# Kernel optimization log

Hardware: AMD Instinct MI355X
Metric: run time of the kernel (lower is better)

The kernel has to match this reference:

```python
import math
import jax, jax.numpy as jnp
import numpy as np

B, S, D, H = 4, 2048, 1024, 16

def setup_inputs() -> dict:
    key = jax.random.key(0)
    k1, k2, k3 = jax.random.split(key, 3)
    scale_in = 1.0 / math.sqrt(D)
    return {
        "x": jax.random.normal(k1, (B, S, D), dtype=jnp.float32),
        "w_in": jax.random.normal(k2, (D, 3 * D), dtype=jnp.float32) * scale_in,
        "b_in": jnp.zeros((3 * D,), dtype=jnp.float32),
        "w_out": jax.random.normal(k3, (D, D), dtype=jnp.float32) * scale_in,
        "b_out": jnp.zeros((D,), dtype=jnp.float32),
    }

def reference(x, w_in, b_in, w_out, b_out):
    b, s, d = x.shape
    hd = d // H  # head dim
    qkv = x @ w_in + b_in                       # [B,S,3D]
    q, k, v = jnp.split(qkv, 3, axis=-1)        # each [B,S,D]
    # [B,H,S,hd]
    q = q.reshape(b, s, H, hd).transpose(0, 2, 1, 3)
    k = k.reshape(b, s, H, hd).transpose(0, 2, 1, 3)
    v = v.reshape(b, s, H, hd).transpose(0, 2, 1, 3)
    attn = jnp.einsum('bhqd,bhkd->bhqk', q, k) / math.sqrt(hd)  # [B,H,S,S]
    causal = jnp.tril(jnp.ones((s, s), dtype=bool))
    attn = jnp.where(causal[None, None], attn, -jnp.inf)
    attn = jax.nn.softmax(attn, axis=-1)
    out = jnp.einsum('bhqk,bhkd->bhqd', attn, v)  # [B,H,S,hd]
    out = out.transpose(0, 2, 1, 3).reshape(b, s, d)
    return out @ w_out + b_out
```

## Files before the change

### kernel.cpp

```cpp
#include <hip/hip_runtime.h>
#include <stdint.h>

#define B_   4
#define S_   2048
#define D_   1024
#define H_   16
#define HD_  64
#define BH_  (B_*H_)
#define M_   (B_*S_)
#define KD_  1024

typedef __bf16 bf16x8 __attribute__((ext_vector_type(8)));
typedef float f32x4 __attribute__((ext_vector_type(4)));
typedef float f32x16 __attribute__((ext_vector_type(16)));
typedef unsigned int u32x4 __attribute__((ext_vector_type(4)));

__device__ __forceinline__ unsigned short f2bf(float f) {
  unsigned int u = __float_as_uint(f);
  u = u + 0x7fffu + ((u >> 16) & 1u);
  return (unsigned short)(u >> 16);
}

__device__ __forceinline__ void gload16(const void* g, void* lds) {
  __builtin_amdgcn_global_load_lds(
      (__attribute__((address_space(1))) void*)(g),
      (__attribute__((address_space(3))) void*)(lds),
      16, 0, 0);
}

__device__ __forceinline__ bf16x8 ldfrag(const unsigned short* p) {
  return *reinterpret_cast<const bf16x8*>(p);
}

__device__ __forceinline__ unsigned int cvtpk(float lo, float hi) {
  unsigned int r;
  asm("v_cvt_pk_bf16_f32 %0, %1, %2" : "=v"(r) : "v"(lo), "v"(hi));
  return r;
}

__device__ __forceinline__ void plswap(unsigned int& a, unsigned int& b) {
  asm("v_permlane32_swap_b32 %0, %1" : "+v"(a), "+v"(b));
}

__device__ __forceinline__ float2 pkadd2(float2 a, float2 b) {
  float2 r;
  asm("v_pk_add_f32 %0, %1, %2" : "=v"(r) : "v"(a), "v"(b));
  return r;
}

__device__ __forceinline__ bf16x8 mkfrag(unsigned int a, unsigned int b,
                                         unsigned int c, unsigned int d) {
  union { unsigned int w[4]; bf16x8 v; } u;
  u.w[0] = a; u.w[1] = b; u.w[2] = c; u.w[3] = d;
  return u.v;
}

__global__ __launch_bounds__(256) void xconv(const float* __restrict__ in,
                                             unsigned short* __restrict__ out) {
  const size_t i = (size_t)blockIdx.x * 256 + threadIdx.x;
  const float4* p = reinterpret_cast<const float4*>(in) + i * 2;
  float4 a = p[0], b = p[1];
  union { u32x4 v; unsigned short u[8]; } cv;
  cv.u[0] = f2bf(a.x); cv.u[1] = f2bf(a.y); cv.u[2] = f2bf(a.z); cv.u[3] = f2bf(a.w);
  cv.u[4] = f2bf(b.x); cv.u[5] = f2bf(b.y); cv.u[6] = f2bf(b.z); cv.u[7] = f2bf(b.w);
  *reinterpret_cast<u32x4*>(out + i * 8) = cv.v;
}

__global__ __launch_bounds__(256) void wtrans(const float* __restrict__ src,
                                              unsigned short* __restrict__ dst,
                                              int R, int C) {
  __shared__ float t[32][33];
  const int c0 = blockIdx.x * 32, r0 = blockIdx.y * 32;
  const int x = threadIdx.x & 31, y = threadIdx.x >> 5;
#pragma unroll
  for (int yy = y; yy < 32; yy += 8)
    t[yy][x] = src[(size_t)(r0 + yy) * C + c0 + x];
  __syncthreads();
#pragma unroll
  for (int yy = y; yy < 32; yy += 8)
    dst[(size_t)(c0 + yy) * R + r0 + x] = f2bf(t[x][yy]);
}

__global__ __launch_bounds__(256) void qkv_gemm(
    const unsigned short* __restrict__ A,
    const unsigned short* __restrict__ Bt,
    const float* __restrict__ bias,
    unsigned short* __restrict__ Qo,
    unsigned short* __restrict__ Ko,
    unsigned short* __restrict__ Vto)
{
  __shared__ unsigned short Al[2][128 * 32];
  __shared__ unsigned short Bl[2][128 * 32];
  const int tid = threadIdx.x;
  const int w = tid >> 6, l = tid & 63;
  const int g = l >> 4, c = l & 15;
  const int m0 = blockIdx.y * 128, n0 = blockIdx.x * 128;
  const int wr = (w >> 1) * 64, wc = (w & 1) * 64;

  f32x4 acc[4][4] = {};

  const int srow = w * 32 + (l >> 2);
  const int slc  = ((l & 3) ^ ((l >> 3) & 3)) * 8;
  const unsigned short* Ag = A  + (size_t)(m0 + srow) * KD_ + slc;
  const unsigned short* Bg = Bt + (size_t)(n0 + srow) * KD_ + slc;

  const int sA = (c >> 1) & 3;

#define GSTAGE(buf, kt) do {                                    \
    gload16(Ag + (kt),            &Al[buf][(w*32)*32]);         \
    gload16(Ag + 16*KD_ + (kt),   &Al[buf][(w*32+16)*32]);      \
    gload16(Bg + (kt),            &Bl[buf][(w*32)*32]);         \
    gload16(Bg + 16*KD_ + (kt),   &Bl[buf][(w*32+16)*32]);      \
  } while (0)

  GSTAGE(0, 0);
  int cur = 0;
  for (int kt = 0; kt < KD_; kt += 32) {
    if (kt + 32 < KD_) {
      GSTAGE(cur ^ 1, kt + 32);
      asm volatile("s_waitcnt vmcnt(4)" ::: "memory");
    } else {
      asm volatile("s_waitcnt vmcnt(0)" ::: "memory");
    }
    __builtin_amdgcn_s_barrier();
    __builtin_amdgcn_sched_barrier(0);
    bf16x8 af[4], bfr[4];
#pragma unroll
    for (int i = 0; i < 4; ++i)
      af[i] = ldfrag(&Al[cur][(wr + i * 16 + c) * 32 + ((g ^ sA) << 3)]);
#pragma unroll
    for (int j = 0; j < 4; ++j)
      bfr[j] = ldfrag(&Bl[cur][(wc + j * 16 + c) * 32 + ((g ^ sA) << 3)]);
#pragma unroll
    for (int i = 0; i < 4; ++i)
#pragma unroll
      for (int j = 0; j < 4; ++j)
        acc[i][j] = __builtin_amdgcn_mfma_f32_16x16x32_bf16(af[i], bfr[j], acc[i][j], 0, 0, 0);
    __builtin_amdgcn_sched_barrier(0);
    __builtin_amdgcn_s_barrier();
    cur ^= 1;
  }
#undef GSTAGE

  if (n0 >= 2048) {
#pragma unroll
    for (int i = 0; i < 4; ++i)
#pragma unroll
      for (int j = 0; j < 4; ++j) {
        const int ng = n0 + wc + j * 16 + c;
        const int n  = ng - 2048;
        const int hh = n >> 6, dim = n & 63;
        const int m  = m0 + wr + i * 16 + g * 4;
        const int bb = m >> 11, ss = m & 2047;
        const float bv = bias[ng];
        uint2 pk;
        pk.x = cvtpk(acc[i][j][0] + bv, acc[i][j][1] + bv);
        pk.y = cvtpk(acc[i][j][2] + bv, acc[i][j][3] + bv);
        *reinterpret_cast<uint2*>(
            &Vto[((size_t)(bb * H_ + hh) * HD_ + dim) * S_ + ss]) = pk;
      }
  } else {
#pragma unroll
    for (int i = 0; i < 4; ++i)
#pragma unroll
      for (int j = 0; j < 4; ++j)
#pragma unroll
        for (int r = 0; r < 4; ++r) {
          const int m = m0 + wr + i * 16 + g * 4 + r;
          const int n = n0 + wc + j * 16 + c;
          float v = acc[i][j][r] + bias[n];
          const int which = n >> 10;
          const int dp = n & 1023;
          const int hh = dp >> 6, dim = dp & 63;
          const int bb = m >> 11, ss = m & 2047;
          const size_t idx = ((size_t)(bb * H_ + hh) * S_ + ss) * HD_ + dim;
          if (which == 0) Qo[idx] = f2bf(v * 0.18033688f);
          else            Ko[idx] = f2bf(v);
        }
  }
}

__global__ __launch_bounds__(256) void out_gemm(
    const unsigned short* __restrict__ A,
    const unsigned short* __restrict__ Bt,
    const float* __restrict__ bias,
    float* __restrict__ C)
{
  __shared__ unsigned short Al[2][128 * 32];
  __shared__ unsigned short Bl[2][128 * 32];
  const int tid = threadIdx.x;
  const int w = tid >> 6, l = tid & 63;
  const int g = l >> 4, c = l & 15;
  const int m0 = blockIdx.y * 128, n0 = blockIdx.x * 128;
  const int wr = (w >> 1) * 64, wc = (w & 1) * 64;

  f32x4 acc[4][4] = {};

  const int srow = w * 32 + (l >> 2);
  const int slc  = ((l & 3) ^ ((l >> 3) & 3)) * 8;
  const unsigned short* Ag = A  + (size_t)(m0 + srow) * KD_ + slc;
  const unsigned short* Bg = Bt + (size_t)(n0 + srow) * KD_ + slc;

  const int sA = (c >> 1) & 3;

#define GSTAGE(buf, kt) do {                                    \
    gload16(Ag + (kt),            &Al[buf][(w*32)*32]);         \
    gload16(Ag + 16*KD_ + (kt),   &Al[buf][(w*32+16)*32]);      \
    gload16(Bg + (kt),            &Bl[buf][(w*32)*32]);         \
    gload16(Bg + 16*KD_ + (kt),   &Bl[buf][(w*32+16)*32]);      \
  } while (0)

  GSTAGE(0, 0);
  int cur = 0;
  for (int kt = 0; kt < KD_; kt += 32) {
    if (kt + 32 < KD_) {
      GSTAGE(cur ^ 1, kt + 32);
      asm volatile("s_waitcnt vmcnt(4)" ::: "memory");
    } else {
      asm volatile("s_waitcnt vmcnt(0)" ::: "memory");
    }
    __builtin_amdgcn_s_barrier();
    __builtin_amdgcn_sched_barrier(0);
    bf16x8 af[4], bfr[4];
#pragma unroll
    for (int i = 0; i < 4; ++i)
      af[i] = ldfrag(&Al[cur][(wr + i * 16 + c) * 32 + ((g ^ sA) << 3)]);
#pragma unroll
    for (int j = 0; j < 4; ++j)
      bfr[j] = ldfrag(&Bl[cur][(wc + j * 16 + c) * 32 + ((g ^ sA) << 3)]);
#pragma unroll
    for (int i = 0; i < 4; ++i)
#pragma unroll
      for (int j = 0; j < 4; ++j)
        acc[i][j] = __builtin_amdgcn_mfma_f32_16x16x32_bf16(af[i], bfr[j], acc[i][j], 0, 0, 0);
    __builtin_amdgcn_sched_barrier(0);
    __builtin_amdgcn_s_barrier();
    cur ^= 1;
  }
#undef GSTAGE

#pragma unroll
  for (int i = 0; i < 4; ++i)
#pragma unroll
    for (int j = 0; j < 4; ++j)
#pragma unroll
      for (int r = 0; r < 4; ++r) {
        const int m = m0 + wr + i * 16 + g * 4 + r;
        const int n = n0 + wc + j * 16 + c;
        C[(size_t)m * D_ + n] = acc[i][j][r] + bias[n];
      }
}

__global__ __launch_bounds__(256) void attn_fwd4(
    const unsigned short* __restrict__ Q,
    const unsigned short* __restrict__ Kg,
    const unsigned short* __restrict__ Vt,
    unsigned short* __restrict__ O)
{
  __shared__ unsigned short Kl[2][64 * 64];
  __shared__ unsigned short Vl[2][64 * 64];

  const int tid = threadIdx.x;
  const int w = tid >> 6, l = tid & 63;
  const int q32 = l & 31, hi = l >> 5;

  const int raw = blockIdx.y * 8 + blockIdx.x;
  const int work = (raw & 7) * 64 + (raw >> 3);
  const int bh = work >> 3;
  const int p  = work & 7;
  const int q0A = p * 128;
  const int q0B = (15 - p) * 128;
  const int nA = 2 * (p + 1);
  const int nB = 2 * (16 - p);
  const int total = nA + nB;

  const unsigned short* Kbh = Kg + (size_t)bh * (S_ * HD_);
  const unsigned short* Vbh = Vt + (size_t)bh * (HD_ * S_);

  bf16x8 qf[4];
  auto loadQ = [&](int q0) {
    const unsigned short* Qrow = Q + ((size_t)bh * S_ + q0 + w * 32 + q32) * HD_ + hi * 8;
#pragma unroll
    for (int s = 0; s < 4; ++s) qf[s] = ldfrag(Qrow + s * 16);
  };

  f32x16 od0 = {}, od1 = {};
  float lrun = 0.f;

  const int krow = w * 16 + (l >> 3);
  const int slc = ((l & 7) ^ (l >> 3)) * 8;

#define LDSOFF(r, ch) ((r) * 64 + (((ch) ^ ((r) & 7)) << 3))

#define STAGE(buf, tile) do {                                                   \
    const int k0s = (tile) * 64;                                                \
    gload16(Kbh + (size_t)(k0s + krow) * HD_ + slc,     &Kl[buf][(w*16)*64]);   \
    gload16(Kbh + (size_t)(k0s + krow + 8) * HD_ + slc, &Kl[buf][(w*16+8)*64]); \
    gload16(Vbh + (size_t)krow * S_ + k0s + slc,        &Vl[buf][(w*16)*64]);   \
    gload16(Vbh + (size_t)(krow + 8) * S_ + k0s + slc,  &Vl[buf][(w*16+8)*64]); \
  } while (0)

  auto epilogue = [&](int q0) {
    const float rl = 1.0f / lrun;
    const int bb = bh >> 4, hh = bh & 15;
    const int sq = q0 + w * 32 + q32;
    unsigned short* Orow = O + ((size_t)bb * S_ + sq) * D_ + hh * HD_;
#pragma unroll
    for (int rr = 0; rr < 4; ++rr) {
      uint2 v0, v1;
      v0.x = cvtpk(od0[4 * rr] * rl,     od0[4 * rr + 1] * rl);
      v0.y = cvtpk(od0[4 * rr + 2] * rl, od0[4 * rr + 3] * rl);
      *reinterpret_cast<uint2*>(Orow + 8 * rr + 4 * hi) = v0;
      v1.x = cvtpk(od1[4 * rr] * rl,     od1[4 * rr + 1] * rl);
      v1.y = cvtpk(od1[4 * rr + 2] * rl, od1[4 * rr + 3] * rl);
      *reinterpret_cast<uint2*>(Orow + 32 + 8 * rr + 4 * hi) = v1;
    }
  };

  loadQ(q0A);
  STAGE(0, 0);
  int cur = 0;
  int q0 = q0A;

  for (int idx = 0; idx < total; ++idx) {
    const bool inA = idx < nA;
    const int kv = inA ? idx : idx - nA;
    const int k0 = kv * 64;
    if (idx + 1 < total) {
      const int nkv = (idx + 1 < nA) ? idx + 1 : idx + 1 - nA;
      STAGE(cur ^ 1, nkv);
      asm volatile("s_waitcnt vmcnt(4)" ::: "memory");
    } else {
      asm volatile("s_waitcnt vmcnt(0)" ::: "memory");
    }
    __builtin_amdgcn_s_barrier();
    __builtin_amdgcn_sched_barrier(0);

    const int wqmin = q0 + w * 32;
    if (k0 <= wqmin + 31) {
      const bool live1 = (k0 + 32 <= wqmin + 31);
      const unsigned short* Kb_ = &Kl[cur][0];
      const unsigned short* Vb_ = &Vl[cur][0];

      f32x16 st0 = {}, st1 = {};
      __builtin_amdgcn_s_setprio(1);
#pragma unroll
      for (int s = 0; s < 4; ++s) {
        bf16x8 kf = ldfrag(Kb_ + LDSOFF(q32, 2 * s + hi));
        st0 = __builtin_amdgcn_mfma_f32_32x32x16_bf16(kf, qf[s], st0, 0, 0, 0);
      }
      if (live1) {
#pragma unroll
        for (int s = 0; s < 4; ++s) {
          bf16x8 kf = ldfrag(Kb_ + LDSOFF(32 + q32, 2 * s + hi));
          st1 = __builtin_amdgcn_mfma_f32_32x32x16_bf16(kf, qf[s], st1, 0, 0, 0);
        }
      }
      __builtin_amdgcn_s_setprio(0);

      if (k0 + 63 > wqmin) {
        const int rel = wqmin + q32 - k0;
#pragma unroll
        for (int r = 0; r < 16; ++r) {
          const int kva = (r & 3) + 8 * (r >> 2) + 4 * hi;
          if (kva > rel) st0[r] = -1e30f;
        }
        if (live1) {
#pragma unroll
          for (int r = 0; r < 16; ++r) {
            const int kva = (r & 3) + 8 * (r >> 2) + 4 * hi;
            if (kva + 32 > rel) st1[r] = -1e30f;
          }
        }
      }

      float2 e0[8], e1[8];
#pragma unroll
      for (int r = 0; r < 8; ++r) {
        e0[r].x = __builtin_amdgcn_exp2f(st0[2 * r]);
        e0[r].y = __builtin_amdgcn_exp2f(st0[2 * r + 1]);
      }
      float2 a0 = pkadd2(pkadd2(e0[0], e0[1]), pkadd2(e0[2], e0[3]));
      float2 a1 = pkadd2(pkadd2(e0[4], e0[5]), pkadd2(e0[6], e0[7]));
      float2 asum = pkadd2(a0, a1);
      if (live1) {
#pragma unroll
        for (int r = 0; r < 8; ++r) {
          e1[r].x = __builtin_amdgcn_exp2f(st1[2 * r]);
          e1[r].y = __builtin_amdgcn_exp2f(st1[2 * r + 1]);
        }
        float2 b0 = pkadd2(pkadd2(e1[0], e1[1]), pkadd2(e1[2], e1[3]));
        float2 b1 = pkadd2(pkadd2(e1[4], e1[5]), pkadd2(e1[6], e1[7]));
        asum = pkadd2(asum, pkadd2(b0, b1));
      }
      float ps = asum.x + asum.y;
      ps += __shfl_xor(ps, 32);
      lrun += ps;

      unsigned int W0, W1, W2, W3, W4, W5, W6, W7;
      W0 = cvtpk(e0[0].x, e0[0].y); W1 = cvtpk(e0[1].x, e0[1].y);
      W2 = cvtpk(e0[2].x, e0[2].y); W3 = cvtpk(e0[3].x, e0[3].y);
      W4 = cvtpk(e0[4].x, e0[4].y); W5 = cvtpk(e0[5].x, e0[5].y);
      W6 = cvtpk(e0[6].x, e0[6].y); W7 = cvtpk(e0[7].x, e0[7].y);
      plswap(W0, W2); plswap(W1, W3); plswap(W4, W6); plswap(W5, W7);
      const bf16x8 pa0 = mkfrag(W0, W1, W2, W3);
      const bf16x8 pa1 = mkfrag(W4, W5, W6, W7);
      bf16x8 pa2, pa3;
      if (live1) {
        W0 = cvtpk(e1[0].x, e1[0].y); W1 = cvtpk(e1[1].x, e1[1].y);
        W2 = cvtpk(e1[2].x, e1[2].y); W3 = cvtpk(e1[3].x, e1[3].y);
        W4 = cvtpk(e1[4].x, e1[4].y); W5 = cvtpk(e1[5].x, e1[5].y);
        W6 = cvtpk(e1[6].x, e1[6].y); W7 = cvtpk(e1[7].x, e1[7].y);
        plswap(W0, W2); plswap(W1, W3); plswap(W4, W6); plswap(W5, W7);
        pa2 = mkfrag(W0, W1, W2, W3);
        pa3 = mkfrag(W4, W5, W6, W7);
      }

      __builtin_amdgcn_s_setprio(1);
#pragma unroll
      for (int s = 0; s < 2; ++s) {
        const bf16x8 pa = (s == 0) ? pa0 : pa1;
        bf16x8 vf = ldfrag(Vb_ + LDSOFF(q32, 2 * s + hi));
        od0 = __builtin_amdgcn_mfma_f32_32x32x16_bf16(vf, pa, od0, 0, 0, 0);
        bf16x8 vg = ldfrag(Vb_ + LDSOFF(32 + q32, 2 * s + hi));
        od1 = __builtin_amdgcn_mfma_f32_32x32x16_bf16(vg, pa, od1, 0, 0, 0);
      }
      if (live1) {
#pragma unroll
        for (int s = 2; s < 4; ++s) {
          const bf16x8 pa = (s == 2) ? pa2 : pa3;
          bf16x8 vf = ldfrag(Vb_ + LDSOFF(q32, 2 * s + hi));
          od0 = __builtin_amdgcn_mfma_f32_32x32x16_bf16(vf, pa, od0, 0, 0, 0);
          bf16x8 vg = ldfrag(Vb_ + LDSOFF(32 + q32, 2 * s + hi));
          od1 = __builtin_amdgcn_mfma_f32_32x32x16_bf16(vg, pa, od1, 0, 0, 0);
        }
      }
      __builtin_amdgcn_s_setprio(0);
    }

    __builtin_amdgcn_sched_barrier(0);
    __builtin_amdgcn_s_barrier();

    if (idx == nA - 1) {
      epilogue(q0A);
      loadQ(q0B);
      od0 = {}; od1 = {};
      lrun = 0.f;
      q0 = q0B;
    }
    cur ^= 1;
  }

  epilogue(q0B);
#undef STAGE
#undef LDSOFF
}

extern "C" void kernel_launch(void* const* d_in, const int* in_sizes, int n_in,
                              void* d_out, int out_size, void* d_ws, size_t ws_size,
                              hipStream_t stream) {
  (void)in_sizes; (void)n_in; (void)out_size; (void)ws_size;
  const float* x     = (const float*)d_in[0];
  const float* w_in  = (const float*)d_in[1];
  const float* b_in  = (const float*)d_in[2];
  const float* w_out = (const float*)d_in[3];
  const float* b_out = (const float*)d_in[4];
  float* out = (float*)d_out;
  char* ws = (char*)d_ws;
  const size_t MB = 1024 * 1024;
  unsigned short* xb     = (unsigned short*)(ws);
  unsigned short* w_inb  = (unsigned short*)(ws + 16 * MB);
  unsigned short* w_outb = (unsigned short*)(ws + 22 * MB);
  unsigned short* Qb     = (unsigned short*)(ws + 24 * MB);
  unsigned short* Kb     = (unsigned short*)(ws + 40 * MB);
  unsigned short* Vt     = (unsigned short*)(ws + 56 * MB);
  unsigned short* Ob     = (unsigned short*)(ws + 72 * MB);

  xconv<<<4096, 256, 0, stream>>>(x, xb);
  wtrans<<<dim3(96, 32), 256, 0, stream>>>(w_in, w_inb, 1024, 3072);
  wtrans<<<dim3(32, 32), 256, 0, stream>>>(w_out, w_outb, 1024, 1024);
  qkv_gemm<<<dim3(24, 64), 256, 0, stream>>>(xb, w_inb, b_in, Qb, Kb, Vt);
  attn_fwd4<<<dim3(8, 64), 256, 0, stream>>>(Qb, Kb, Vt, Ob);
  out_gemm<<<dim3(8, 64), 256, 0, stream>>>(Ob, w_outb, b_out, out);
}
```

Baseline: 172.1 us.

## Fuse prep kernels and remap GEMM tiles for XCD-aware L2 locality

Merges the x conversion and the two weight transposes into one prep launch, cutting two kernel launches. Remaps the QKV GEMM's flat block index so that each XCD (blockIdx mod 8) handles a contiguous set of three N-columns of w_in, which should improve per-XCD L2 reuse of weight tiles. The output GEMM moves to a flat 1D grid with N varying fastest. The prep kernel now reserves shared memory even for its conversion blocks, which may limit their occupancy slightly.

After: 175.3 us. No clear change (+1.9%).

```diff
diff --git a/kernel.cpp b/kernel.cpp
--- a/kernel.cpp
+++ b/kernel.cpp
@@ -55,30 +55,41 @@
   return u.v;
 }
 
-__global__ __launch_bounds__(256) void xconv(const float* __restrict__ in,
-                                             unsigned short* __restrict__ out) {
-  const size_t i = (size_t)blockIdx.x * 256 + threadIdx.x;
-  const float4* p = reinterpret_cast<const float4*>(in) + i * 2;
-  float4 a = p[0], b = p[1];
-  union { u32x4 v; unsigned short u[8]; } cv;
-  cv.u[0] = f2bf(a.x); cv.u[1] = f2bf(a.y); cv.u[2] = f2bf(a.z); cv.u[3] = f2bf(a.w);
-  cv.u[4] = f2bf(b.x); cv.u[5] = f2bf(b.y); cv.u[6] = f2bf(b.z); cv.u[7] = f2bf(b.w);
-  *reinterpret_cast<u32x4*>(out + i * 8) = cv.v;
-}
-
-__global__ __launch_bounds__(256) void wtrans(const float* __restrict__ src,
-                                              unsigned short* __restrict__ dst,
-                                              int R, int C) {
+__global__ __launch_bounds__(256) void prep(
+    const float* __restrict__ x,     unsigned short* __restrict__ xb,
+    const float* __restrict__ w_in,  unsigned short* __restrict__ w_inb,
+    const float* __restrict__ w_out, unsigned short* __restrict__ w_outb) {
+  const int bid = blockIdx.x;
+  const int tid = threadIdx.x;
+  if (bid < 4096) {
+    const size_t i = (size_t)bid * 256 + tid;
+    const float4* p = reinterpret_cast<const float4*>(x) + i * 2;
+    float4 a = p[0], b = p[1];
+    union { u32x4 v; unsigned short u[8]; } cv;
+    cv.u[0] = f2bf(a.x); cv.u[1] = f2bf(a.y); cv.u[2] = f2bf(a.z); cv.u[3] = f2bf(a.w);
+    cv.u[4] = f2bf(b.x); cv.u[5] = f2bf(b.y); cv.u[6] = f2bf(b.z); cv.u[7] = f2bf(b.w);
+    *reinterpret_cast<u32x4*>(xb + i * 8) = cv.v;
+    return;
+  }
   __shared__ float t[32][33];
-  const int c0 = blockIdx.x * 32, r0 = blockIdx.y * 32;
-  const int x = threadIdx.x & 31, y = threadIdx.x >> 5;
-#pragma unroll
-  for (int yy = y; yy < 32; yy += 8)
-    t[yy][x] = src[(size_t)(r0 + yy) * C + c0 + x];
+  const float* src; unsigned short* dst; int R, C, c0, r0;
+  if (bid < 7168) {
+    const int b = bid - 4096;
+    src = w_in; dst = w_inb; R = 1024; C = 3072;
+    c0 = (b % 96) * 32; r0 = (b / 96) * 32;
+  } else {
+    const int b = bid - 7168;
+    src = w_out; dst = w_outb; R = 1024; C = 1024;
+    c0 = (b % 32) * 32; r0 = (b / 32) * 32;
+  }
+  const int xx = tid & 31, yy = tid >> 5;
+#pragma unroll
+  for (int y2 = yy; y2 < 32; y2 += 8)
+    t[y2][xx] = src[(size_t)(r0 + y2) * C + c0 + xx];
   __syncthreads();
 #pragma unroll
-  for (int yy = y; yy < 32; yy += 8)
-    dst[(size_t)(c0 + yy) * R + r0 + x] = f2bf(t[x][yy]);
+  for (int y2 = yy; y2 < 32; y2 += 8)
+    dst[(size_t)(c0 + y2) * R + r0 + xx] = f2bf(t[xx][y2]);
 }
 
 __global__ __launch_bounds__(256) void qkv_gemm(
@@ -94,7 +105,10 @@
   const int tid = threadIdx.x;
   const int w = tid >> 6, l = tid & 63;
   const int g = l >> 4, c = l & 15;
-  const int m0 = blockIdx.y * 128, n0 = blockIdx.x * 128;
+  const int flat = blockIdx.x;
+  const int xcd = flat & 7, rr_ = flat >> 3;
+  const int n0 = (xcd * 3 + (rr_ >> 6)) * 128;
+  const int m0 = (rr_ & 63) * 128;
   const int wr = (w >> 1) * 64, wc = (w & 1) * 64;
 
   f32x4 acc[4][4] = {};
@@ -191,7 +205,9 @@
   const int tid = threadIdx.x;
   const int w = tid >> 6, l = tid & 63;
   const int g = l >> 4, c = l & 15;
-  const int m0 = blockIdx.y * 128, n0 = blockIdx.x * 128;
+  const int flat = blockIdx.x;
+  const int n0 = (flat & 7) * 128;
+  const int m0 = (flat >> 3) * 128;
   const int wr = (w >> 1) * 64, wc = (w & 1) * 64;
 
   f32x4 acc[4][4] = {};
@@ -476,10 +492,8 @@
   unsigned short* Vt     = (unsigned short*)(ws + 56 * MB);
   unsigned short* Ob     = (unsigned short*)(ws + 72 * MB);
 
-  xconv<<<4096, 256, 0, stream>>>(x, xb);
-  wtrans<<<dim3(96, 32), 256, 0, stream>>>(w_in, w_inb, 1024, 3072);
-  wtrans<<<dim3(32, 32), 256, 0, stream>>>(w_out, w_outb, 1024, 1024);
-  qkv_gemm<<<dim3(24, 64), 256, 0, stream>>>(xb, w_inb, b_in, Qb, Kb, Vt);
+  prep<<<8192, 256, 0, stream>>>(x, xb, w_in, w_inb, w_out, w_outb);
+  qkv_gemm<<<1536, 256, 0, stream>>>(xb, w_inb, b_in, Qb, Kb, Vt);
   attn_fwd4<<<dim3(8, 64), 256, 0, stream>>>(Qb, Kb, Vt, Ob);
-  out_gemm<<<dim3(8, 64), 256, 0, stream>>>(Ob, w_outb, b_out, out);
-}
+  out_gemm<<<512, 256, 0, stream>>>(Ob, w_outb, b_out, out);
+}
```
